# Kernel tuning notes

Hardware: AMD Instinct MI355X
Metric: run time of the kernel (lower is better)

Reference implementation:

```python
import jax, jax.numpy as jnp
import numpy as np

TAU = 0.5
EPS = 1e-08
NORM_EPS = 1e-12  # F.normalize clamp

BS = 4096
D = 256


def _l2_normalize(x):
    n = jnp.linalg.norm(x, axis=1, keepdims=True)
    return x / jnp.maximum(n, NORM_EPS)


def setup_inputs() -> dict:
    key = jax.random.key(0)
    k1, k2 = jax.random.split(key)
    zi = jax.random.normal(k1, (BS, D), dtype=jnp.float32)
    zj = jax.random.normal(k2, (BS, D), dtype=jnp.float32)
    return {"zi": zi, "zj": zj}


def reference(zi, zj):
    bs = zi.shape[0]
    zi_n = _l2_normalize(zi)
    zj_n = _l2_normalize(zj)
    z = jnp.concatenate([zi_n, zj_n], axis=0)  # [2bs, d]
    # cosine sim of unit vectors == dot product
    sim = (z @ z.T) / TAU  # [2bs, 2bs]
    # positive pairs: (i, i+bs) and (i+bs, i) -> same diag values twice
    pos_diag = jnp.sum(zi_n * zj_n, axis=1) / TAU  # [bs]
    sim_pos = jnp.exp(jnp.concatenate([pos_diag, pos_diag]))  # [2bs]
    # negatives: all off-diagonal entries per row
    exp_sim = jnp.exp(sim)
    neg_sum = jnp.sum(exp_sim, axis=1) - jnp.diagonal(exp_sim)  # [2bs]
    loss = jnp.mean(-jnp.log(sim_pos / (neg_sum + EPS)))
    return loss
```

## Files before the change

### kernel.cpp

```cpp
#include <hip/hip_runtime.h>

#define N_TOT 8192
#define BSZ   4096
#define DIM   256

typedef __attribute__((ext_vector_type(4)))  float f32x4;
typedef __attribute__((ext_vector_type(16))) float f32x16;
typedef __attribute__((ext_vector_type(4)))  int   i32x4;
typedef __attribute__((ext_vector_type(8)))  int   i32x8;

#define PRESCALE 1.69864362f
#define SCALE1   0x7F7F7F7F

__device__ __forceinline__ void async_copy16(const void* g, void* l) {
    __builtin_amdgcn_global_load_lds((const __attribute__((address_space(1))) void*)g,
                                     (__attribute__((address_space(3))) void*)l,
                                     16, 0, 0);
}

__global__ __launch_bounds__(256) void norm_kernel(const float* __restrict__ zi,
                                                   const float* __restrict__ zj,
                                                   unsigned char* __restrict__ zb,
                                                   float* __restrict__ posPart) {
    __shared__ float buf[2][256];
    const int wid  = threadIdx.x >> 6;
    const int lane = threadIdx.x & 63;
    const int pair = blockIdx.x * 2 + (wid & 1);
    const bool isZj = (wid >= 2);
    const float* src = isZj ? (zj + (size_t)pair * DIM) : (zi + (size_t)pair * DIM);
    float4 v = ((const float4*)src)[lane];
    float ss = v.x * v.x + v.y * v.y + v.z * v.z + v.w * v.w;
    #pragma unroll
    for (int off = 1; off < 64; off <<= 1) ss += __shfl_xor(ss, off);
    float inv = 1.0f / fmaxf(sqrtf(ss), 1e-12f);
    float4 nv = make_float4(v.x * inv, v.y * inv, v.z * inv, v.w * inv);

    const int outRow = isZj ? (pair + BSZ) : pair;
    int pk = __builtin_amdgcn_cvt_pk_fp8_f32(nv.x * PRESCALE, nv.y * PRESCALE, 0, false);
    pk     = __builtin_amdgcn_cvt_pk_fp8_f32(nv.z * PRESCALE, nv.w * PRESCALE, pk, true);
    *(int*)(zb + (size_t)outRow * 256 + lane * 4) = pk;

    if (!isZj) ((float4*)&buf[wid & 1][0])[lane] = nv;
    __syncthreads();
    if (isZj) {
        float4 a = ((float4*)&buf[wid & 1][0])[lane];
        float d = a.x * nv.x + a.y * nv.y + a.z * nv.z + a.w * nv.w;
        #pragma unroll
        for (int off = 1; off < 64; off <<= 1) d += __shfl_xor(d, off);
        if (lane == 0) posPart[pair] = d;
    }
}

__global__ __launch_bounds__(256, 4) void sim_kernel(const unsigned char* __restrict__ zb,
                                                     float* __restrict__ partial) {
    __shared__ alignas(16) char smem[32768];

    const int t    = threadIdx.x;
    const int lane = t & 63;
    const int wid  = t >> 6;
    const int wr   = wid >> 1;
    const int wc   = wid & 1;
    const int hi   = lane >> 5;
    const int r31  = lane & 31;

    const int k = blockIdx.x;
    int bi = (int)((129.0f - sqrtf(16641.0f - 8.0f * (float)k)) * 0.5f);
    while (bi * 64 - bi * (bi - 1) / 2 > k) bi--;
    while ((bi + 1) * 64 - (bi + 1) * bi / 2 <= k) bi++;
    const int bj = bi + (k - (bi * 64 - bi * (bi - 1) / 2));
    const bool diag = (bi == bj);

    const int row0 = bi * 128;
    const int col0 = bj * 128;

    f32x16 acc[2][2];
    #pragma unroll
    for (int mt = 0; mt < 2; mt++)
        #pragma unroll
        for (int nt = 0; nt < 2; nt++)
            #pragma unroll
            for (int r = 0; r < 16; r++) acc[mt][nt][r] = 0.f;

    #define STAGE(b, kt) do {                                                   \
        _Pragma("unroll")                                                       \
        for (int i = 0; i < 2; i++) {                                           \
            const int e_  = i * 256 + t;                   \
            const int rr_ = e_ >> 2;                       \
            const int p_  = e_ & 3;                             \
            const int g_  = p_ ^ ((rr_ >> 2) & 3);           \
            char* lb = smem + (b) * 16384 + (i * 256 + wid * 64) * 16;          \
            async_copy16(zb + (size_t)(row0 + rr_) * 256 + (kt) * 64 + g_ * 16, \
                         lb);                                                   \
            async_copy16(zb + (size_t)(col0 + rr_) * 256 + (kt) * 64 + g_ * 16, \
                         lb + 8192);                                            \
        } } while (0)

    STAGE(0, 0);

    #pragma unroll
    for (int kt = 0; kt < 4; ++kt) {
        const int cur = kt & 1;
        if (kt < 3) {
            STAGE(cur ^ 1, kt + 1);
            asm volatile("s_waitcnt vmcnt(4)" ::: "memory");
        } else {
            asm volatile("s_waitcnt vmcnt(0)" ::: "memory");
        }
        __builtin_amdgcn_sched_barrier(0);
        __builtin_amdgcn_s_barrier();

        const char* Ab = smem + cur * 16384;
        const char* Bb = Ab + 8192;
        i32x8 af[2], bfr[2];
        #pragma unroll
        for (int mt = 0; mt < 2; mt++) {
            const int rr = wr * 64 + mt * 32 + r31;
            const int s  = (rr >> 2) & 3;
            i32x4 lo = *(const i32x4*)(Ab + rr * 64 + ((hi * 2)     ^ s) * 16);
            i32x4 hv = *(const i32x4*)(Ab + rr * 64 + ((hi * 2 + 1) ^ s) * 16);
            af[mt] = __builtin_shufflevector(lo, hv, 0, 1, 2, 3, 4, 5, 6, 7);
        }
        #pragma unroll
        for (int nt = 0; nt < 2; nt++) {
            const int rr = wc * 64 + nt * 32 + r31;
            const int s  = (rr >> 2) & 3;
            i32x4 lo = *(const i32x4*)(Bb + rr * 64 + ((hi * 2)     ^ s) * 16);
            i32x4 hv = *(const i32x4*)(Bb + rr * 64 + ((hi * 2 + 1) ^ s) * 16);
            bfr[nt] = __builtin_shufflevector(lo, hv, 0, 1, 2, 3, 4, 5, 6, 7);
        }
        #pragma unroll
        for (int mt = 0; mt < 2; mt++)
            #pragma unroll
            for (int nt = 0; nt < 2; nt++)
                acc[mt][nt] = __builtin_amdgcn_mfma_scale_f32_32x32x64_f8f6f4(
                    af[mt], bfr[nt], acc[mt][nt], 0, 0, 0, SCALE1, 0, SCALE1);

        __builtin_amdgcn_sched_barrier(0);
        __builtin_amdgcn_s_barrier();
    }
    #undef STAGE

    float* sw = (float*)smem + wid * 2048;
    float csum[2] = {0.f, 0.f};

    #pragma unroll
    for (int mt = 0; mt < 2; mt++) {
        #pragma unroll
        for (int reg = 0; reg < 16; reg++) {
            const int row_l = mt * 32 + (reg & 3) + ((reg >> 2) << 3) + (hi << 2);
            const int rowg  = row0 + wr * 64 + row_l;
            float r = 0.f;
            #pragma unroll
            for (int nt = 0; nt < 2; nt++) {
                float e = exp2f(acc[mt][nt][reg]);
                if (diag && rowg == (col0 + wc * 64 + nt * 32 + r31)) e = 0.0f;
                r += e;
                csum[nt] += e;
            }
            sw[row_l * 32 + ((((r31 >> 2) ^ (row_l & 7))) << 2) + (r31 & 3)] = r;
        }
    }

    if (!diag) {
        float cv0 = csum[0] + __shfl_xor(csum[0], 32);
        float cv1 = csum[1] + __shfl_xor(csum[1], 32);
        const float cv = hi ? cv1 : cv0;
        partial[(size_t)(bi * 2 + wr) * N_TOT + col0 + wc * 64 + lane] = cv;
    }

    asm volatile("s_waitcnt lgkmcnt(0)" ::: "memory");
    __builtin_amdgcn_sched_barrier(0);
    float tot = 0.f;
    #pragma unroll
    for (int q = 0; q < 8; q++) {
        const int ch = q ^ (lane & 7);
        f32x4 v = *(const f32x4*)(sw + lane * 32 + ch * 4);
        tot += v[0] + v[1] + v[2] + v[3];
    }
    partial[(size_t)(bj * 2 + wc) * N_TOT + row0 + wr * 64 + lane] = tot;
}

__global__ __launch_bounds__(256) void rowlog_kernel(const float* __restrict__ partial,
                                                     float* __restrict__ logPart) {
    const int lane = threadIdx.x & 63;
    const int w    = threadIdx.x >> 6;
    const int row  = blockIdx.x * 64 + lane;
    float s = 0.f;
    #pragma unroll 8
    for (int p = w * 32; p < w * 32 + 32; p++) s += partial[(size_t)p * N_TOT + row];
    __shared__ float red[4][64];
    red[w][lane] = s;
    __syncthreads();
    if (w == 0) {
        float tot = red[0][lane] + red[1][lane] + red[2][lane] + red[3][lane];
        float v = logf(tot + 1e-8f);
        #pragma unroll
        for (int off = 1; off < 64; off <<= 1) v += __shfl_xor(v, off);
        if (lane == 0) logPart[blockIdx.x] = v;
    }
}

__global__ __launch_bounds__(256) void final_kernel(const float* __restrict__ logPart,
                                                    const float* __restrict__ posPart,
                                                    float* __restrict__ out) {
    const int t = threadIdx.x;
    float ps = 0.f;
    for (int i = t; i < BSZ; i += 256) ps += posPart[i];
    float ls = (t < 128) ? logPart[t] : 0.f;
    #pragma unroll
    for (int off = 1; off < 64; off <<= 1) {
        ps += __shfl_xor(ps, off);
        ls += __shfl_xor(ls, off);
    }
    __shared__ float redp[4], redl[4];
    const int lane = t & 63, wid = t >> 6;
    if (lane == 0) { redp[wid] = ps; redl[wid] = ls; }
    __syncthreads();
    if (t == 0) {
        const float posSum = redp[0] + redp[1] + redp[2] + redp[3];
        const float logSum = redl[0] + redl[1] + redl[2] + redl[3];
        out[0] = logSum / (float)N_TOT - 2.0f * posSum / (float)BSZ;
    }
}

extern "C" void kernel_launch(void* const* d_in, const int* in_sizes, int n_in,
                              void* d_out, int out_size, void* d_ws, size_t ws_size,
                              hipStream_t stream) {
    const float* zi = (const float*)d_in[0];
    const float* zj = (const float*)d_in[1];
    float* out = (float*)d_out;

    char* ws = (char*)d_ws;
    unsigned char* zb = (unsigned char*)ws;
    float* partial     = (float*)(ws + (size_t)(4 << 20));
    float* logPart     = (float*)(ws + (size_t)(8 << 20));
    float* posPart     = (float*)(ws + (size_t)(8 << 20) + 4096);

    norm_kernel<<<2048, 256, 0, stream>>>(zi, zj, zb, posPart);
    sim_kernel<<<2080, 256, 0, stream>>>(zb, partial);
    rowlog_kernel<<<128, 256, 0, stream>>>(partial, logPart);
    final_kernel<<<1, 256, 0, stream>>>(logPart, posPart, out);
}
```

Before: 38.63 us.

## Give each wave its own 64x64 tile with direct global-to-register loads

The sim kernel now assigns an independent 64x64 upper-triangular tile to each wave, 8256 tiles in total, instead of one 128x128 tile per block. Operand fragments are loaded straight from global memory into registers with double buffering, which removes the LDS staging, the async copies and the block barriers. The cost is less operand reuse, so global and L2 traffic roughly doubles, and the partial buffer now holds 128 row-block partials, which rowlog still sums. Occupancy is lowered to 3 blocks per SM to allow more registers.

```diff
diff --git a/kernel.cpp b/kernel.cpp
--- a/kernel.cpp
+++ b/kernel.cpp
@@ -11,12 +11,6 @@
 
 #define PRESCALE 1.69864362f
 #define SCALE1   0x7F7F7F7F
-
-__device__ __forceinline__ void async_copy16(const void* g, void* l) {
-    __builtin_amdgcn_global_load_lds((const __attribute__((address_space(1))) void*)g,
-                                     (__attribute__((address_space(3))) void*)l,
-                                     16, 0, 0);
-}
 
 __global__ __launch_bounds__(256) void norm_kernel(const float* __restrict__ zi,
                                                    const float* __restrict__ zj,
@@ -51,27 +45,30 @@
     }
 }
 
-__global__ __launch_bounds__(256, 4) void sim_kernel(const unsigned char* __restrict__ zb,
+__global__ __launch_bounds__(256, 3) void sim_kernel(const unsigned char* __restrict__ zb,
                                                      float* __restrict__ partial) {
-    __shared__ alignas(16) char smem[32768];
+    __shared__ float swAll[4][2048];
 
     const int t    = threadIdx.x;
     const int lane = t & 63;
     const int wid  = t >> 6;
-    const int wr   = wid >> 1;
-    const int wc   = wid & 1;
     const int hi   = lane >> 5;
     const int r31  = lane & 31;
 
-    const int k = blockIdx.x;
-    int bi = (int)((129.0f - sqrtf(16641.0f - 8.0f * (float)k)) * 0.5f);
-    while (bi * 64 - bi * (bi - 1) / 2 > k) bi--;
-    while ((bi + 1) * 64 - (bi + 1) * bi / 2 <= k) bi++;
-    const int bj = bi + (k - (bi * 64 - bi * (bi - 1) / 2));
+    const int k = blockIdx.x * 4 + wid;
+    int bi = (int)((257.0f - sqrtf(fmaxf(66049.0f - 8.0f * (float)k, 0.f))) * 0.5f);
+    if (bi < 0) bi = 0; if (bi > 127) bi = 127;
+    while (bi > 0 && (bi * 257 - bi * bi) / 2 > k) bi--;
+    while (((bi + 1) * 257 - (bi + 1) * (bi + 1)) / 2 <= k) bi++;
+    const int bj = bi + (k - (bi * 257 - bi * bi) / 2);
     const bool diag = (bi == bj);
-
-    const int row0 = bi * 128;
-    const int col0 = bj * 128;
+    const int row0 = bi * 64;
+    const int col0 = bj * 64;
+
+    const unsigned char* A0 = zb + (size_t)(row0 + r31) * 256 + hi * 32;
+    const unsigned char* A1 = A0 + 32 * 256;
+    const unsigned char* B0 = zb + (size_t)(col0 + r31) * 256 + hi * 32;
+    const unsigned char* B1 = B0 + 32 * 256;
 
     f32x16 acc[2][2];
     #pragma unroll
@@ -81,66 +78,41 @@
             #pragma unroll
             for (int r = 0; r < 16; r++) acc[mt][nt][r] = 0.f;
 
-    #define STAGE(b, kt) do {                                                   \
-        _Pragma("unroll")                                                       \
-        for (int i = 0; i < 2; i++) {                                           \
-            const int e_  = i * 256 + t;                   \
-            const int rr_ = e_ >> 2;                       \
-            const int p_  = e_ & 3;                             \
-            const int g_  = p_ ^ ((rr_ >> 2) & 3);           \
-            char* lb = smem + (b) * 16384 + (i * 256 + wid * 64) * 16;          \
-            async_copy16(zb + (size_t)(row0 + rr_) * 256 + (kt) * 64 + g_ * 16, \
-                         lb);                                                   \
-            async_copy16(zb + (size_t)(col0 + rr_) * 256 + (kt) * 64 + g_ * 16, \
-                         lb + 8192);                                            \
-        } } while (0)
-
-    STAGE(0, 0);
+    i32x4 aL[2][2], aH[2][2], bL[2][2], bH[2][2];
+
+    #define LOADF(b, kt) do {                                                   \
+        aL[b][0] = *(const i32x4*)(A0 + (kt) * 64);                             \
+        aH[b][0] = *(const i32x4*)(A0 + (kt) * 64 + 16);                        \
+        aL[b][1] = *(const i32x4*)(A1 + (kt) * 64);                             \
+        aH[b][1] = *(const i32x4*)(A1 + (kt) * 64 + 16);                        \
+        bL[b][0] = *(const i32x4*)(B0 + (kt) * 64);                             \
+        bH[b][0] = *(const i32x4*)(B0 + (kt) * 64 + 16);                        \
+        bL[b][1] = *(const i32x4*)(B1 + (kt) * 64);                             \
+        bH[b][1] = *(const i32x4*)(B1 + (kt) * 64 + 16);                        \
+    } while (0)
+
+    LOADF(0, 0);
 
     #pragma unroll
     for (int kt = 0; kt < 4; ++kt) {
         const int cur = kt & 1;
-        if (kt < 3) {
-            STAGE(cur ^ 1, kt + 1);
-            asm volatile("s_waitcnt vmcnt(4)" ::: "memory");
-        } else {
-            asm volatile("s_waitcnt vmcnt(0)" ::: "memory");
+        if (kt < 3) LOADF(cur ^ 1, kt + 1);
+        #pragma unroll
+        for (int mt = 0; mt < 2; mt++) {
+            const i32x8 a = __builtin_shufflevector(aL[cur][mt], aH[cur][mt],
+                                                    0, 1, 2, 3, 4, 5, 6, 7);
+            #pragma unroll
+            for (int nt = 0; nt < 2; nt++) {
+                const i32x8 b = __builtin_shufflevector(bL[cur][nt], bH[cur][nt],
+                                                        0, 1, 2, 3, 4, 5, 6, 7);
+                acc[mt][nt] = __builtin_amdgcn_mfma_scale_f32_32x32x64_f8f6f4(
+                    a, b, acc[mt][nt], 0, 0, 0, SCALE1, 0, SCALE1);
+            }
         }
-        __builtin_amdgcn_sched_barrier(0);
-        __builtin_amdgcn_s_barrier();
-
-        const char* Ab = smem + cur * 16384;
-        const char* Bb = Ab + 8192;
-        i32x8 af[2], bfr[2];
-        #pragma unroll
-        for (int mt = 0; mt < 2; mt++) {
-            const int rr = wr * 64 + mt * 32 + r31;
-            const int s  = (rr >> 2) & 3;
-            i32x4 lo = *(const i32x4*)(Ab + rr * 64 + ((hi * 2)     ^ s) * 16);
-            i32x4 hv = *(const i32x4*)(Ab + rr * 64 + ((hi * 2 + 1) ^ s) * 16);
-            af[mt] = __builtin_shufflevector(lo, hv, 0, 1, 2, 3, 4, 5, 6, 7);
-        }
-        #pragma unroll
-        for (int nt = 0; nt < 2; nt++) {
-            const int rr = wc * 64 + nt * 32 + r31;
-            const int s  = (rr >> 2) & 3;
-            i32x4 lo = *(const i32x4*)(Bb + rr * 64 + ((hi * 2)     ^ s) * 16);
-            i32x4 hv = *(const i32x4*)(Bb + rr * 64 + ((hi * 2 + 1) ^ s) * 16);
-            bfr[nt] = __builtin_shufflevector(lo, hv, 0, 1, 2, 3, 4, 5, 6, 7);
-        }
-        #pragma unroll
-        for (int mt = 0; mt < 2; mt++)
-            #pragma unroll
-            for (int nt = 0; nt < 2; nt++)
-                acc[mt][nt] = __builtin_amdgcn_mfma_scale_f32_32x32x64_f8f6f4(
-                    af[mt], bfr[nt], acc[mt][nt], 0, 0, 0, SCALE1, 0, SCALE1);
-
-        __builtin_amdgcn_sched_barrier(0);
-        __builtin_amdgcn_s_barrier();
-    }
-    #undef STAGE
-
-    float* sw = (float*)smem + wid * 2048;
+    }
+    #undef LOADF
+
+    float* sw = swAll[wid];
     float csum[2] = {0.f, 0.f};
 
     #pragma unroll
@@ -148,12 +120,12 @@
         #pragma unroll
         for (int reg = 0; reg < 16; reg++) {
             const int row_l = mt * 32 + (reg & 3) + ((reg >> 2) << 3) + (hi << 2);
-            const int rowg  = row0 + wr * 64 + row_l;
+            const int rowg  = row0 + row_l;
             float r = 0.f;
             #pragma unroll
             for (int nt = 0; nt < 2; nt++) {
                 float e = exp2f(acc[mt][nt][reg]);
-                if (diag && rowg == (col0 + wc * 64 + nt * 32 + r31)) e = 0.0f;
+                if (diag && rowg == (col0 + nt * 32 + r31)) e = 0.0f;
                 r += e;
                 csum[nt] += e;
             }
@@ -165,7 +137,7 @@
         float cv0 = csum[0] + __shfl_xor(csum[0], 32);
         float cv1 = csum[1] + __shfl_xor(csum[1], 32);
         const float cv = hi ? cv1 : cv0;
-        partial[(size_t)(bi * 2 + wr) * N_TOT + col0 + wc * 64 + lane] = cv;
+        partial[(size_t)bi * N_TOT + col0 + lane] = cv;
     }
 
     asm volatile("s_waitcnt lgkmcnt(0)" ::: "memory");
@@ -177,7 +149,7 @@
         f32x4 v = *(const f32x4*)(sw + lane * 32 + ch * 4);
         tot += v[0] + v[1] + v[2] + v[3];
     }
-    partial[(size_t)(bj * 2 + wc) * N_TOT + row0 + wr * 64 + lane] = tot;
+    partial[(size_t)bj * N_TOT + row0 + lane] = tot;
 }
 
 __global__ __launch_bounds__(256) void rowlog_kernel(const float* __restrict__ partial,
@@ -237,7 +209,7 @@
     float* posPart     = (float*)(ws + (size_t)(8 << 20) + 4096);
 
     norm_kernel<<<2048, 256, 0, stream>>>(zi, zj, zb, posPart);
-    sim_kernel<<<2080, 256, 0, stream>>>(zb, partial);
+    sim_kernel<<<2064, 256, 0, stream>>>(zb, partial);
     rowlog_kernel<<<128, 256, 0, stream>>>(partial, logPart);
     final_kernel<<<1, 256, 0, stream>>>(logPart, posPart, out);
 }
```

Result: slower. 55.03 us (+42.4%).
